# Kernel tuning notes

Hardware: AMD Instinct MI355X
Metric: run time of the kernel (lower is better)

Reference implementation:

```python
import jax, jax.numpy as jnp
import numpy as np

VOXEL_W, VOXEL_H, VOXEL_D = 60, 36, 60
V = VOXEL_W * VOXEL_H * VOXEL_D  # 129600


def setup_inputs() -> dict:
    key = jax.random.key(0)
    k1, k2 = jax.random.split(key)
    features_2d = jax.random.normal(k1, (4, 128, 240, 320), dtype=jnp.float32)
    projection_indices = jax.random.randint(k2, (240, 320), 0, V, dtype=jnp.int64)
    return {"features_2d": features_2d, "projection_indices": projection_indices}


def reference(features_2d, projection_indices):
    B, C, H, W = features_2d.shape
    feat_flat = features_2d.reshape(B, C, H * W)          # [B, C, HW]
    proj_flat = projection_indices.reshape(-1)            # [HW]
    # Single fused scatter-add over all (B, C) slices: indices broadcast on
    # the last axis, so one scatter covers the whole [B, C, HW] update.
    out_flat = jnp.zeros((B, C, V), dtype=features_2d.dtype)
    out_flat = out_flat.at[:, :, proj_flat].add(feat_flat)
    return out_flat.reshape(B, C, VOXEL_W, VOXEL_H, VOXEL_D)
```

## Files before the change

kernel.cpp:

```cpp
#include <hip/hip_runtime.h>


static constexpr int HW = 240 * 320;
static constexpr int V  = 60 * 36 * 60;
static constexpr int B  = 4;
static constexpr int C  = 128;
static constexpr int BC = B * C;
static constexpr int NBV = (V + 255) / 256;
static constexpr int NHWT = HW / 64;
static constexpr int NBCT = BC / 64;
static constexpr int VT = 16;
static constexpr int NVT = V / VT;
static constexpr int SMP = BC + 1;

typedef float f4 __attribute__((ext_vector_type(4)));

static __device__ __forceinline__ unsigned short f2bf(float x) {
    unsigned int u = __builtin_bit_cast(unsigned int, x);
    unsigned int r = (u + 0x7FFFu + ((u >> 16) & 1u)) >> 16;
    return (unsigned short)r;
}
static __device__ __forceinline__ float bf2f(unsigned short s) {
    unsigned int u = ((unsigned int)s) << 16;
    return __builtin_bit_cast(float, u);
}

__global__ void __launch_bounds__(256) zero_kernel(int* __restrict__ cnt) {
    int i = blockIdx.x * 256 + threadIdx.x;
    if (i < V) cnt[i] = 0;
}

__global__ void __launch_bounds__(256) count_kernel(const int* __restrict__ idx,
                                                    int* __restrict__ cnt) {
    int hw = blockIdx.x * 256 + threadIdx.x;
    if (hw < HW) atomicAdd(&cnt[idx[hw]], 1);
}

__global__ void __launch_bounds__(256) blocksum_kernel(const int* __restrict__ cnt,
                                                       int* __restrict__ bsum) {
    int i = blockIdx.x * 256 + threadIdx.x;
    int v = (i < V) ? cnt[i] : 0;
#pragma unroll
    for (int d = 32; d > 0; d >>= 1) v += __shfl_down(v, d, 64);
    __shared__ int ws[4];
    if ((threadIdx.x & 63) == 0) ws[threadIdx.x >> 6] = v;
    __syncthreads();
    if (threadIdx.x == 0) bsum[blockIdx.x] = ws[0] + ws[1] + ws[2] + ws[3];
}

__global__ void __launch_bounds__(512) scan_bsum_kernel(int* __restrict__ bsum) {
    __shared__ int sm[512];
    int t = threadIdx.x;
    int v = (t < NBV) ? bsum[t] : 0;
    sm[t] = v;
    __syncthreads();
    for (int d = 1; d < 512; d <<= 1) {
        int x = (t >= d) ? sm[t - d] : 0;
        __syncthreads();
        sm[t] += x;
        __syncthreads();
    }
    if (t < NBV) bsum[t] = sm[t] - v;
}

__global__ void __launch_bounds__(256) scatter_off_kernel(int* __restrict__ cnt,
                                                          const int* __restrict__ bsum,
                                                          int* __restrict__ cursor) {
    int i = blockIdx.x * 256 + threadIdx.x;
    int c = (i < V) ? cnt[i] : 0;
    int lane = threadIdx.x & 63, w = threadIdx.x >> 6;
    int inc = c;
#pragma unroll
    for (int d = 1; d < 64; d <<= 1) {
        int x = __shfl_up(inc, d, 64);
        if (lane >= d) inc += x;
    }
    __shared__ int wsum[4];
    if (lane == 63) wsum[w] = inc;
    __syncthreads();
    int woff = 0;
    for (int k = 0; k < w; ++k) woff += wsum[k];
    int excl = inc - c + woff + bsum[blockIdx.x];
    if (i < V) { cnt[i] = excl; cursor[i] = excl; }
    if (i == 0) cnt[V] = HW;
}

__global__ void __launch_bounds__(256) rank_kernel(const int* __restrict__ idx,
                                                   int* __restrict__ cursor,
                                                   int* __restrict__ rank) {
    int hw = blockIdx.x * 256 + threadIdx.x;
    if (hw < HW) {
        int v = idx[hw];
        rank[hw] = atomicAdd(&cursor[v], 1);
    }
}

__global__ void __launch_bounds__(256) transpose_perm_kernel(
        const float* __restrict__ feat, const int* __restrict__ rank,
        unsigned short* __restrict__ featP) {
    __shared__ float tile[64][65];
    __shared__ int rk[64];
    int hw0 = blockIdx.x * 64;
    int bc0 = blockIdx.y * 64;
    int t   = threadIdx.x;

    if (t < 64) rk[t] = rank[hw0 + t];

    {
        int cq = t & 15;
        int r0 = t >> 4;
#pragma unroll
        for (int k = 0; k < 4; ++k) {
            int r = r0 + 16 * k;
            f4 v = *(const f4*)(feat + (long long)(bc0 + r) * HW + hw0 + 4 * cq);
            tile[r][4 * cq + 0] = v.x;
            tile[r][4 * cq + 1] = v.y;
            tile[r][4 * cq + 2] = v.z;
            tile[r][4 * cq + 3] = v.w;
        }
    }
    __syncthreads();

    {
        int q  = t & 7;
        int h0 = t >> 3;
#pragma unroll
        for (int k = 0; k < 2; ++k) {
            int h = h0 + 32 * k;
            int dst = rk[h];
            union { unsigned short us[8]; uint4 v; } p;
#pragma unroll
            for (int i = 0; i < 8; ++i)
                p.us[i] = f2bf(tile[8 * q + i][h]);
            *(uint4*)(featP + (long long)dst * BC + bc0 + 8 * q) = p.v;
        }
    }
}

__global__ void __launch_bounds__(512) gatherT_kernel(
        const unsigned short* __restrict__ featP, const int* __restrict__ off,
        float* __restrict__ out) {
    __shared__ float sm[VT][SMP];
    int v0 = blockIdx.x * VT;
    int t = threadIdx.x;
    float acc[VT];
    int jprev = off[v0];
#pragma unroll
    for (int i = 0; i < VT; ++i) {
        int j1 = off[v0 + i + 1];
        float a = 0.f;
        for (int j = jprev; j < j1; ++j)
            a += bf2f(featP[(long long)j * BC + t]);
        acc[i] = a;
        jprev = j1;
    }
#pragma unroll
    for (int i = 0; i < VT; ++i) sm[i][t] = acc[i];
    __syncthreads();

#pragma unroll
    for (int r = 0; r < 4; ++r) {
        int e  = r * 512 + t;
        int bc = e >> 2;
        int vq = e & 3;
        f4 val = { sm[vq * 4 + 0][bc], sm[vq * 4 + 1][bc],
                   sm[vq * 4 + 2][bc], sm[vq * 4 + 3][bc] };
        __builtin_nontemporal_store(val, (f4*)(out + (long long)bc * V + v0 + vq * 4));
    }
}

static constexpr int BCPT = 8;
static constexpr int NG = BC / BCPT;
static constexpr int NXCD = 8;
static constexpr int GPX = NG / NXCD;

__global__ void __launch_bounds__(256) perm_kernel(const int* __restrict__ idx,
                                                   int* __restrict__ cursor,
                                                   int* __restrict__ perm) {
    int hw = blockIdx.x * 256 + threadIdx.x;
    if (hw < HW) {
        int v = idx[hw];
        int pos = atomicAdd(&cursor[v], 1);
        perm[pos] = hw;
    }
}

__global__ void __launch_bounds__(256) gather_kernel(const float* __restrict__ feat,
                                                     const int* __restrict__ off,
                                                     const int* __restrict__ perm,
                                                     float* __restrict__ out) {
    int bid  = blockIdx.x;
    int xcd  = bid & (NXCD - 1);
    int lid  = bid >> 3;
    int gloc = lid / NBV;
    int vblk = lid - gloc * NBV;
    int g    = xcd * GPX + gloc;
    int v    = vblk * 256 + threadIdx.x;
    if (v >= V) return;
    int bc0 = g * BCPT;
    int j0 = off[v];
    int j1 = off[v + 1];
    const float* f = feat + (long long)bc0 * HW;
    float s[BCPT];
#pragma unroll
    for (int k = 0; k < BCPT; ++k) s[k] = 0.f;
    for (int j = j0; j < j1; ++j) {
        int p = perm[j];
#pragma unroll
        for (int k = 0; k < BCPT; ++k) s[k] += f[p + k * HW];
    }
    long long o = (long long)bc0 * V + v;
#pragma unroll
    for (int k = 0; k < BCPT; ++k)
        __builtin_nontemporal_store(s[k], &out[o + (long long)k * V]);
}

extern "C" void kernel_launch(void* const* d_in, const int* in_sizes, int n_in,
                              void* d_out, int out_size, void* d_ws, size_t ws_size,
                              hipStream_t stream) {
    const float* feat = (const float*)d_in[0];
    const int*   idx  = (const int*)d_in[1];
    float*       out  = (float*)d_out;

    int* off    = (int*)d_ws;
    int* cursor = off + (V + 1);
    int* rank   = cursor + V;
    int* bsum   = rank + HW;
    size_t hdr_bytes = ((size_t)(V + 1 + V + HW + 512) * 4 + 255) & ~(size_t)255;
    unsigned short* featP = (unsigned short*)((char*)d_ws + hdr_bytes);
    size_t need = hdr_bytes + (size_t)HW * BC * sizeof(unsigned short);

    zero_kernel       <<<NBV, 256, 0, stream>>>(off);
    count_kernel      <<<(HW + 255) / 256, 256, 0, stream>>>(idx, off);
    blocksum_kernel   <<<NBV, 256, 0, stream>>>(off, bsum);
    scan_bsum_kernel  <<<1, 512, 0, stream>>>(bsum);
    scatter_off_kernel<<<NBV, 256, 0, stream>>>(off, bsum, cursor);

    if (ws_size >= need) {
        rank_kernel<<<(HW + 255) / 256, 256, 0, stream>>>(idx, cursor, rank);
        dim3 tgrid(NHWT, NBCT);
        transpose_perm_kernel<<<tgrid, 256, 0, stream>>>(feat, rank, featP);
        gatherT_kernel<<<NVT, 512, 0, stream>>>(featP, off, out);
    } else {
        perm_kernel<<<(HW + 255) / 256, 256, 0, stream>>>(idx, cursor, rank);
        gather_kernel<<<NXCD * GPX * NBV, 256, 0, stream>>>(feat, off, rank, out);
    }
}
```

Baseline: 143.1 us.

## Fuse rank assignment into transpose and retile gather over voxel and channel blocks

The rank kernel is folded into the transpose kernel: each block atomically claims slots for its 64 pixels and then loops over all channel tiles itself, so one kernel launch and one pass over the rank array go away. The gather kernel is retiled into 160-voxel by 64-channel blocks, with each wave summing a run of voxels. This gives longer contiguous output rows of 640 bytes per channel instead of 64, and a 2D grid with an occupancy hint. The trade-off is a much smaller transpose grid (1200 blocks that loop serially over channel tiles) and gather reads of only 128 bytes per row of the bf16 buffer, which may hurt coalescing.

```diff
diff --git a/kernel.cpp b/kernel.cpp
--- a/kernel.cpp
+++ b/kernel.cpp
@@ -8,10 +8,12 @@
 static constexpr int BC = B * C;
 static constexpr int NBV = (V + 255) / 256;
 static constexpr int NHWT = HW / 64;
-static constexpr int NBCT = BC / 64;
-static constexpr int VT = 16;
-static constexpr int NVT = V / VT;
-static constexpr int SMP = BC + 1;
+
+static constexpr int VT   = 160;
+static constexpr int BCB  = 64;
+static constexpr int NGX  = V / VT;
+static constexpr int NGY  = BC / BCB;
+static constexpr int VPG  = VT / 8;
 
 typedef float f4 __attribute__((ext_vector_type(4)));
 
@@ -85,87 +87,80 @@
     if (i == 0) cnt[V] = HW;
 }
 
-__global__ void __launch_bounds__(256) rank_kernel(const int* __restrict__ idx,
-                                                   int* __restrict__ cursor,
-                                                   int* __restrict__ rank) {
-    int hw = blockIdx.x * 256 + threadIdx.x;
-    if (hw < HW) {
-        int v = idx[hw];
-        rank[hw] = atomicAdd(&cursor[v], 1);
-    }
-}
-
-__global__ void __launch_bounds__(256) transpose_perm_kernel(
-        const float* __restrict__ feat, const int* __restrict__ rank,
-        unsigned short* __restrict__ featP) {
+__global__ void __launch_bounds__(512) transpose_perm_kernel(
+        const float* __restrict__ feat, const int* __restrict__ idx,
+        int* __restrict__ cursor, unsigned short* __restrict__ featP) {
     __shared__ float tile[64][65];
     __shared__ int rk[64];
     int hw0 = blockIdx.x * 64;
-    int bc0 = blockIdx.y * 64;
     int t   = threadIdx.x;
 
-    if (t < 64) rk[t] = rank[hw0 + t];
-
-    {
-        int cq = t & 15;
-        int r0 = t >> 4;
-#pragma unroll
-        for (int k = 0; k < 4; ++k) {
-            int r = r0 + 16 * k;
+    if (t < 64) {
+        int v = idx[hw0 + t];
+        rk[t] = atomicAdd(&cursor[v], 1);
+    }
+
+    for (int by = 0; by < NGY; ++by) {
+        int bc0 = by * 64;
+#pragma unroll
+        for (int k = 0; k < 2; ++k) {
+            int u  = k * 512 + t;
+            int r  = u >> 4;
+            int cq = u & 15;
             f4 v = *(const f4*)(feat + (long long)(bc0 + r) * HW + hw0 + 4 * cq);
             tile[r][4 * cq + 0] = v.x;
             tile[r][4 * cq + 1] = v.y;
             tile[r][4 * cq + 2] = v.z;
             tile[r][4 * cq + 3] = v.w;
         }
-    }
-    __syncthreads();
-
-    {
-        int q  = t & 7;
-        int h0 = t >> 3;
-#pragma unroll
-        for (int k = 0; k < 2; ++k) {
-            int h = h0 + 32 * k;
-            int dst = rk[h];
-            union { unsigned short us[8]; uint4 v; } p;
+        __syncthreads();
+        {
+            int h = t >> 3;
+            int q = t & 7;
+            union { unsigned short us[8]; uint4 v4; } p;
 #pragma unroll
             for (int i = 0; i < 8; ++i)
                 p.us[i] = f2bf(tile[8 * q + i][h]);
-            *(uint4*)(featP + (long long)dst * BC + bc0 + 8 * q) = p.v;
+            *(uint4*)(featP + (long long)rk[h] * BC + bc0 + 8 * q) = p.v4;
         }
-    }
-}
-
-__global__ void __launch_bounds__(512) gatherT_kernel(
+        __syncthreads();
+    }
+}
+
+__global__ void __launch_bounds__(512, 6) gatherT_kernel(
         const unsigned short* __restrict__ featP, const int* __restrict__ off,
         float* __restrict__ out) {
-    __shared__ float sm[VT][SMP];
-    int v0 = blockIdx.x * VT;
-    int t = threadIdx.x;
-    float acc[VT];
-    int jprev = off[v0];
-#pragma unroll
-    for (int i = 0; i < VT; ++i) {
-        int j1 = off[v0 + i + 1];
+    __shared__ float sm[VT][BCB + 1];
+    int v0  = blockIdx.x * VT;
+    int bc0 = blockIdx.y * BCB;
+    int t   = threadIdx.x;
+    int bcl = t & 63;
+    int grp = t >> 6;
+    int vb  = grp * VPG;
+
+    float acc[VPG];
+#pragma unroll
+    for (int i = 0; i < VPG; ++i) {
+        int j0 = off[v0 + vb + i];
+        int j1 = off[v0 + vb + i + 1];
         float a = 0.f;
-        for (int j = jprev; j < j1; ++j)
-            a += bf2f(featP[(long long)j * BC + t]);
+        for (int j = j0; j < j1; ++j)
+            a += bf2f(featP[(long long)j * BC + bc0 + bcl]);
         acc[i] = a;
-        jprev = j1;
-    }
-#pragma unroll
-    for (int i = 0; i < VT; ++i) sm[i][t] = acc[i];
-    __syncthreads();
-
-#pragma unroll
-    for (int r = 0; r < 4; ++r) {
-        int e  = r * 512 + t;
-        int bc = e >> 2;
-        int vq = e & 3;
-        f4 val = { sm[vq * 4 + 0][bc], sm[vq * 4 + 1][bc],
-                   sm[vq * 4 + 2][bc], sm[vq * 4 + 3][bc] };
-        __builtin_nontemporal_store(val, (f4*)(out + (long long)bc * V + v0 + vq * 4));
+    }
+#pragma unroll
+    for (int i = 0; i < VPG; ++i) sm[vb + i][bcl] = acc[i];
+    __syncthreads();
+
+#pragma unroll
+    for (int w = 0; w < 5; ++w) {
+        int u = w * 512 + t;
+        int r = u / 40;
+        int k = u % 40;
+        f4 val = { sm[4 * k + 0][r], sm[4 * k + 1][r],
+                   sm[4 * k + 2][r], sm[4 * k + 3][r] };
+        __builtin_nontemporal_store(val,
+            (f4*)(out + (long long)(bc0 + r) * V + v0 + 4 * k));
     }
 }
 
@@ -224,8 +219,8 @@
 
     int* off    = (int*)d_ws;
     int* cursor = off + (V + 1);
-    int* rank   = cursor + V;
-    int* bsum   = rank + HW;
+    int* perm   = cursor + V;
+    int* bsum   = perm + HW;
     size_t hdr_bytes = ((size_t)(V + 1 + V + HW + 512) * 4 + 255) & ~(size_t)255;
     unsigned short* featP = (unsigned short*)((char*)d_ws + hdr_bytes);
     size_t need = hdr_bytes + (size_t)HW * BC * sizeof(unsigned short);
@@ -237,12 +232,11 @@
     scatter_off_kernel<<<NBV, 256, 0, stream>>>(off, bsum, cursor);
 
     if (ws_size >= need) {
-        rank_kernel<<<(HW + 255) / 256, 256, 0, stream>>>(idx, cursor, rank);
-        dim3 tgrid(NHWT, NBCT);
-        transpose_perm_kernel<<<tgrid, 256, 0, stream>>>(feat, rank, featP);
-        gatherT_kernel<<<NVT, 512, 0, stream>>>(featP, off, out);
+        transpose_perm_kernel<<<NHWT, 512, 0, stream>>>(feat, idx, cursor, featP);
+        dim3 ggrid(NGX, NGY);
+        gatherT_kernel<<<ggrid, 512, 0, stream>>>(featP, off, out);
     } else {
-        perm_kernel<<<(HW + 255) / 256, 256, 0, stream>>>(idx, cursor, rank);
-        gather_kernel<<<NXCD * GPX * NBV, 256, 0, stream>>>(feat, off, rank, out);
-    }
-}
+        perm_kernel<<<(HW + 255) / 256, 256, 0, stream>>>(idx, cursor, perm);
+        gather_kernel<<<NXCD * GPX * NBV, 256, 0, stream>>>(feat, off, perm, out);
+    }
+}
```

New measurement: 165.9 us. +15.9%, slower.

## Fuse block-prefix scan into offset kernel and rank atomics into transpose

Applied to the files above, without the earlier changes.

Removes the single-block scan kernel by having each scatter_off block sum all preceding block totals itself. It also drops the separate rank kernel: the transpose kernel now takes the atomic slot per pixel directly and loops over all channel tiles within one block, with 512 threads, instead of using a 2D grid. This cuts two launches and the rank buffer round trip. In exchange, every offset block redundantly reads up to 507 block sums, and the transpose grid shrinks to 1200 blocks, each running a serial 8-step loop.

```diff
diff --git a/kernel.cpp b/kernel.cpp
--- a/kernel.cpp
+++ b/kernel.cpp
@@ -8,7 +8,7 @@
 static constexpr int BC = B * C;
 static constexpr int NBV = (V + 255) / 256;
 static constexpr int NHWT = HW / 64;
-static constexpr int NBCT = BC / 64;
+static constexpr int NGY  = BC / 64;
 static constexpr int VT = 16;
 static constexpr int NVT = V / VT;
 static constexpr int SMP = BC + 1;
@@ -48,27 +48,24 @@
     if (threadIdx.x == 0) bsum[blockIdx.x] = ws[0] + ws[1] + ws[2] + ws[3];
 }
 
-__global__ void __launch_bounds__(512) scan_bsum_kernel(int* __restrict__ bsum) {
-    __shared__ int sm[512];
-    int t = threadIdx.x;
-    int v = (t < NBV) ? bsum[t] : 0;
-    sm[t] = v;
-    __syncthreads();
-    for (int d = 1; d < 512; d <<= 1) {
-        int x = (t >= d) ? sm[t - d] : 0;
-        __syncthreads();
-        sm[t] += x;
-        __syncthreads();
-    }
-    if (t < NBV) bsum[t] = sm[t] - v;
-}
-
 __global__ void __launch_bounds__(256) scatter_off_kernel(int* __restrict__ cnt,
                                                           const int* __restrict__ bsum,
                                                           int* __restrict__ cursor) {
-    int i = blockIdx.x * 256 + threadIdx.x;
+    int t = threadIdx.x;
+    int i = blockIdx.x * 256 + t;
+
+    int pre = 0;
+    for (int u = t; u < NBV; u += 256)
+        if (u < blockIdx.x) pre += bsum[u];
+#pragma unroll
+    for (int d = 32; d > 0; d >>= 1) pre += __shfl_down(pre, d, 64);
+    __shared__ int ps[4];
+    if ((t & 63) == 0) ps[t >> 6] = pre;
+    __syncthreads();
+    int blockoff = ps[0] + ps[1] + ps[2] + ps[3];
+
     int c = (i < V) ? cnt[i] : 0;
-    int lane = threadIdx.x & 63, w = threadIdx.x >> 6;
+    int lane = t & 63, w = t >> 6;
     int inc = c;
 #pragma unroll
     for (int d = 1; d < 64; d <<= 1) {
@@ -80,60 +77,48 @@
     __syncthreads();
     int woff = 0;
     for (int k = 0; k < w; ++k) woff += wsum[k];
-    int excl = inc - c + woff + bsum[blockIdx.x];
+    int excl = inc - c + woff + blockoff;
     if (i < V) { cnt[i] = excl; cursor[i] = excl; }
     if (i == 0) cnt[V] = HW;
 }
 
-__global__ void __launch_bounds__(256) rank_kernel(const int* __restrict__ idx,
-                                                   int* __restrict__ cursor,
-                                                   int* __restrict__ rank) {
-    int hw = blockIdx.x * 256 + threadIdx.x;
-    if (hw < HW) {
-        int v = idx[hw];
-        rank[hw] = atomicAdd(&cursor[v], 1);
-    }
-}
-
-__global__ void __launch_bounds__(256) transpose_perm_kernel(
-        const float* __restrict__ feat, const int* __restrict__ rank,
-        unsigned short* __restrict__ featP) {
+__global__ void __launch_bounds__(512) transpose_perm_kernel(
+        const float* __restrict__ feat, const int* __restrict__ idx,
+        int* __restrict__ cursor, unsigned short* __restrict__ featP) {
     __shared__ float tile[64][65];
     __shared__ int rk[64];
     int hw0 = blockIdx.x * 64;
-    int bc0 = blockIdx.y * 64;
     int t   = threadIdx.x;
 
-    if (t < 64) rk[t] = rank[hw0 + t];
-
-    {
-        int cq = t & 15;
-        int r0 = t >> 4;
-#pragma unroll
-        for (int k = 0; k < 4; ++k) {
-            int r = r0 + 16 * k;
+    if (t < 64) {
+        int v = idx[hw0 + t];
+        rk[t] = atomicAdd(&cursor[v], 1);
+    }
+
+    for (int by = 0; by < NGY; ++by) {
+        int bc0 = by * 64;
+#pragma unroll
+        for (int k = 0; k < 2; ++k) {
+            int u  = k * 512 + t;
+            int r  = u >> 4;
+            int cq = u & 15;
             f4 v = *(const f4*)(feat + (long long)(bc0 + r) * HW + hw0 + 4 * cq);
             tile[r][4 * cq + 0] = v.x;
             tile[r][4 * cq + 1] = v.y;
             tile[r][4 * cq + 2] = v.z;
             tile[r][4 * cq + 3] = v.w;
         }
-    }
-    __syncthreads();
-
-    {
-        int q  = t & 7;
-        int h0 = t >> 3;
-#pragma unroll
-        for (int k = 0; k < 2; ++k) {
-            int h = h0 + 32 * k;
-            int dst = rk[h];
-            union { unsigned short us[8]; uint4 v; } p;
+        __syncthreads();
+        {
+            int h = t >> 3;
+            int q = t & 7;
+            union { unsigned short us[8]; uint4 v4; } p;
 #pragma unroll
             for (int i = 0; i < 8; ++i)
                 p.us[i] = f2bf(tile[8 * q + i][h]);
-            *(uint4*)(featP + (long long)dst * BC + bc0 + 8 * q) = p.v;
+            *(uint4*)(featP + (long long)rk[h] * BC + bc0 + 8 * q) = p.v4;
         }
+        __syncthreads();
     }
 }
 
@@ -224,8 +209,8 @@
 
     int* off    = (int*)d_ws;
     int* cursor = off + (V + 1);
-    int* rank   = cursor + V;
-    int* bsum   = rank + HW;
+    int* perm   = cursor + V;
+    int* bsum   = perm + HW;
     size_t hdr_bytes = ((size_t)(V + 1 + V + HW + 512) * 4 + 255) & ~(size_t)255;
     unsigned short* featP = (unsigned short*)((char*)d_ws + hdr_bytes);
     size_t need = hdr_bytes + (size_t)HW * BC * sizeof(unsigned short);
@@ -233,16 +218,13 @@
     zero_kernel       <<<NBV, 256, 0, stream>>>(off);
     count_kernel      <<<(HW + 255) / 256, 256, 0, stream>>>(idx, off);
     blocksum_kernel   <<<NBV, 256, 0, stream>>>(off, bsum);
-    scan_bsum_kernel  <<<1, 512, 0, stream>>>(bsum);
     scatter_off_kernel<<<NBV, 256, 0, stream>>>(off, bsum, cursor);
 
     if (ws_size >= need) {
-        rank_kernel<<<(HW + 255) / 256, 256, 0, stream>>>(idx, cursor, rank);
-        dim3 tgrid(NHWT, NBCT);
-        transpose_perm_kernel<<<tgrid, 256, 0, stream>>>(feat, rank, featP);
+        transpose_perm_kernel<<<NHWT, 512, 0, stream>>>(feat, idx, cursor, featP);
         gatherT_kernel<<<NVT, 512, 0, stream>>>(featP, off, out);
     } else {
-        perm_kernel<<<(HW + 255) / 256, 256, 0, stream>>>(idx, cursor, rank);
-        gather_kernel<<<NXCD * GPX * NBV, 256, 0, stream>>>(feat, off, rank, out);
-    }
-}
+        perm_kernel<<<(HW + 255) / 256, 256, 0, stream>>>(idx, cursor, perm);
+        gather_kernel<<<NXCD * GPX * NBV, 256, 0, stream>>>(feat, off, perm, out);
+    }
+}
```

Result: faster. 138.6 us (median of 2 runs) (-3.2%).
